# Kernel optimization log

Measured on AMD Instinct MI355X. Metric: run time of the kernel, lower is better.

The kernel has to match this reference:

```python
import jax, jax.numpy as jnp
import numpy as np


def setup_inputs() -> dict:
    key = jax.random.key(0)
    ks = jax.random.split(key, 5)
    B, T, S, D = 4, 32, 320, 768
    return {
        "x": jax.random.normal(ks[0], (B, T, S, D), dtype=jnp.float32),
        "qkv_w": jax.random.normal(ks[1], (D, 3 * D), dtype=jnp.float32) * 0.02,
        "qkv_b": jax.random.normal(ks[2], (3 * D,), dtype=jnp.float32) * 0.02,
        "out_w": jax.random.normal(ks[3], (D, D), dtype=jnp.float32) * 0.02,
        "out_b": jax.random.normal(ks[4], (D,), dtype=jnp.float32) * 0.02,
        "n_latents": 64,
        "n_heads": 12,
    }


def reference(x, qkv_w, qkv_b, out_w, out_b, n_latents, n_heads):
    B, T, S, D = x.shape
    H = n_heads
    hd = D // H
    scale = 1.0 / jnp.sqrt(jnp.asarray(hd, dtype=x.dtype))

    # qkv projection: [B,T,S,3D]
    qkv = jnp.einsum('btsd,de->btse', x, qkv_w) + qkv_b
    q, k, v = jnp.split(qkv, 3, axis=-1)
    # [B,T,S,H,hd]
    q = q.reshape(B, T, S, H, hd)
    k = k.reshape(B, T, S, H, hd)
    v = v.reshape(B, T, S, H, hd)

    # block-sparse mask: latent queries (rows < n_latents) cannot attend to
    # patch keys (cols >= n_latents); everything else allowed
    rows = jnp.arange(S) < n_latents          # latent query rows
    cols = jnp.arange(S) >= n_latents         # patch key cols
    allow = ~(rows[:, None] & cols[None, :])  # [S,S] bool

    # attention scores [B,T,H,Sq,Sk]
    scores = jnp.einsum('btqhd,btkhd->bthqk', q, k) * scale
    scores = jnp.where(allow, scores, -jnp.inf)
    attn = jax.nn.softmax(scores, axis=-1)

    y = jnp.einsum('bthqk,btkhd->btqhd', attn, v).reshape(B, T, S, D)
    return jnp.einsum('btsd,de->btse', y, out_w) + out_b
```

## Files before the change

### kernel.cpp

```cpp
#include <hip/hip_runtime.h>

typedef __attribute__((ext_vector_type(8))) short bf16x8;
typedef __attribute__((ext_vector_type(4))) float f32x4;
typedef __attribute__((ext_vector_type(16))) float f32x16;
typedef __attribute__((address_space(1))) void gvoid_t;
typedef __attribute__((address_space(3))) void lvoid_t;

#define DEVI __device__ __forceinline__

DEVI unsigned short f2bf(float f) {
    unsigned int u = __builtin_bit_cast(unsigned int, f);
    u += 0x7fffu + ((u >> 16) & 1u);
    return (unsigned short)(u >> 16);
}

DEVI unsigned cvt_pk_bf16(float a, float b) {
    unsigned r;
    asm("v_cvt_pk_bf16_f32 %0, %1, %2" : "=v"(r) : "v"(a), "v"(b));
    return r;
}

DEVI f32x4 mfma16(bf16x8 a, bf16x8 b, f32x4 c) {
    return __builtin_amdgcn_mfma_f32_16x16x32_bf16(a, b, c, 0, 0, 0);
}

__global__ void k_convert(const float* __restrict__ in, unsigned short* __restrict__ out, int n8) {
    int i = blockIdx.x * 256 + threadIdx.x;
    if (i >= n8) return;
    const float4* p = (const float4*)in + (size_t)i * 2;
    float4 a = p[0], b = p[1];
    uint4 o;
    o.x = f2bf(a.x) | ((unsigned)f2bf(a.y) << 16);
    o.y = f2bf(a.z) | ((unsigned)f2bf(a.w) << 16);
    o.z = f2bf(b.x) | ((unsigned)f2bf(b.y) << 16);
    o.w = f2bf(b.z) | ((unsigned)f2bf(b.w) << 16);
    *((uint4*)out + i) = o;
}

__global__ void k_transpose(const float* __restrict__ w, unsigned short* __restrict__ wt, int K, int N) {
    __shared__ float tile[32][33];
    int n0 = blockIdx.x * 32, k0 = blockIdx.y * 32;
    int tx = threadIdx.x, ty = threadIdx.y;
#pragma unroll
    for (int r = 0; r < 32; r += 8)
        tile[ty + r][tx] = w[(size_t)(k0 + ty + r) * N + n0 + tx];
    __syncthreads();
#pragma unroll
    for (int r = 0; r < 32; r += 8)
        wt[(size_t)(n0 + ty + r) * K + k0 + tx] = f2bf(tile[tx][ty + r]);
}

template <bool OUT_BF16>
__global__ __launch_bounds__(512, 2) void k_gemm256(const unsigned short* __restrict__ A,
                                                    const unsigned short* __restrict__ Bt,
                                                    const float* __restrict__ bias,
                                                    void* __restrict__ out,
                                                    int M, int N, int K) {
    __shared__ unsigned short smem[65536];

    const int tid = threadIdx.x;
    const int nwg = gridDim.x, bid = blockIdx.x;
    const int q8 = nwg >> 3, r8 = nwg & 7;
    const int xcd = bid & 7, lid = bid >> 3;
    const int swz = ((xcd < r8) ? xcd * (q8 + 1) : r8 * (q8 + 1) + (xcd - r8) * q8) + lid;
    const int ntn = N >> 8;
    const int bm = swz / ntn, bn = swz % ntn;

    const int lane = tid & 63, wid = tid >> 6;
    const int wr = wid >> 2, wc = wid & 3;
    const int lr = lane & 15, lg = lane >> 4;
    const int cswz = (lr & 7) << 3;
    const int col0 = (lg * 8) ^ cswz;

    const int NT = K >> 6;

    const int srowl = tid >> 3;
    const int scole = ((tid & 7) ^ (srowl & 7)) << 3;
    const unsigned short* aSrc = A  + (size_t)(bm * 256 + srowl) * K + scole;
    const unsigned short* bSrc = Bt + (size_t)(bn * 256 + srowl) * K + scole;

#define STG(matOff, srcBase, qq, koff, bufw)                                              \
    __builtin_amdgcn_global_load_lds((gvoid_t*)((srcBase) + (size_t)(qq) * 64 * K + (koff)), \
        (lvoid_t*)(smem + (matOff) + (bufw) * 16384 + (qq) * 4096 + tid * 8), 16, 0, 0)

    f32x4 acc[8][4];
#pragma unroll
    for (int i = 0; i < 8; ++i)
#pragma unroll
        for (int j = 0; j < 4; ++j) acc[i][j] = (f32x4){0.f, 0.f, 0.f, 0.f};

    {
        const int k1 = (NT > 1) ? 64 : 0;
        STG(0, aSrc, 0, 0, 0); STG(0, aSrc, 1, 0, 0); STG(0, aSrc, 2, 0, 0); STG(0, aSrc, 3, 0, 0);
        STG(32768, bSrc, 0, 0, 0); STG(32768, bSrc, 1, 0, 0); STG(32768, bSrc, 2, 0, 0); STG(32768, bSrc, 3, 0, 0);
        STG(0, aSrc, 0, k1, 1); STG(0, aSrc, 2, k1, 1);
        asm volatile("s_waitcnt vmcnt(2)" ::: "memory");
        __builtin_amdgcn_s_barrier();
    }

#pragma unroll 1
    for (int t = 0; t < NT; ++t) {
        const int bufR = t & 1, bufW = bufR ^ 1;
        const int ko1 = (t + 1 < NT) ? (t + 1) * 64 : 0;
        const int ko2 = (t + 2 < NT) ? (t + 2) * 64 : 0;
        const unsigned short* abuf = smem + bufR * 16384;
        const unsigned short* bbuf = smem + 32768 + bufR * 16384;
        bf16x8 af[4][2], bfr[2][2];

#pragma unroll
        for (int mf = 0; mf < 4; ++mf)
#pragma unroll
            for (int kk = 0; kk < 2; ++kk)
                af[mf][kk] = *(const bf16x8*)(abuf + (wr * 128 + mf * 16 + lr) * 64 + (col0 ^ (kk * 32)));
#pragma unroll
        for (int j = 0; j < 2; ++j)
#pragma unroll
            for (int kk = 0; kk < 2; ++kk)
                bfr[j][kk] = *(const bf16x8*)(bbuf + (wc * 64 + j * 16 + lr) * 64 + (col0 ^ (kk * 32)));
        STG(32768, bSrc, 0, ko1, bufW); STG(32768, bSrc, 1, ko1, bufW);
        __builtin_amdgcn_s_barrier();
        asm volatile("s_waitcnt lgkmcnt(0)" ::: "memory");
        __builtin_amdgcn_sched_barrier(0);
        __builtin_amdgcn_s_setprio(1);
#pragma unroll
        for (int mf = 0; mf < 4; ++mf)
#pragma unroll
            for (int j = 0; j < 2; ++j)
#pragma unroll
                for (int kk = 0; kk < 2; ++kk)
                    acc[mf][j] = mfma16(af[mf][kk], bfr[j][kk], acc[mf][j]);
        __builtin_amdgcn_s_setprio(0);
        __builtin_amdgcn_s_barrier();

#pragma unroll
        for (int j = 0; j < 2; ++j)
#pragma unroll
            for (int kk = 0; kk < 2; ++kk)
                bfr[j][kk] = *(const bf16x8*)(bbuf + (wc * 64 + (2 + j) * 16 + lr) * 64 + (col0 ^ (kk * 32)));
        STG(32768, bSrc, 2, ko1, bufW); STG(32768, bSrc, 3, ko1, bufW);
        __builtin_amdgcn_s_barrier();
        asm volatile("s_waitcnt lgkmcnt(0)" ::: "memory");
        __builtin_amdgcn_sched_barrier(0);
        __builtin_amdgcn_s_setprio(1);
#pragma unroll
        for (int mf = 0; mf < 4; ++mf)
#pragma unroll
            for (int j = 0; j < 2; ++j)
#pragma unroll
                for (int kk = 0; kk < 2; ++kk)
                    acc[mf][2 + j] = mfma16(af[mf][kk], bfr[j][kk], acc[mf][2 + j]);
        __builtin_amdgcn_s_setprio(0);
        __builtin_amdgcn_s_barrier();

#pragma unroll
        for (int mf = 0; mf < 4; ++mf)
#pragma unroll
            for (int kk = 0; kk < 2; ++kk)
                af[mf][kk] = *(const bf16x8*)(abuf + (wr * 128 + 64 + mf * 16 + lr) * 64 + (col0 ^ (kk * 32)));
        STG(0, aSrc, 1, ko1, bufW); STG(0, aSrc, 3, ko1, bufW);
        __builtin_amdgcn_s_barrier();
        asm volatile("s_waitcnt lgkmcnt(0)" ::: "memory");
        __builtin_amdgcn_sched_barrier(0);
        __builtin_amdgcn_s_setprio(1);
#pragma unroll
        for (int mf = 0; mf < 4; ++mf)
#pragma unroll
            for (int j = 0; j < 2; ++j)
#pragma unroll
                for (int kk = 0; kk < 2; ++kk)
                    acc[4 + mf][2 + j] = mfma16(af[mf][kk], bfr[j][kk], acc[4 + mf][2 + j]);
        __builtin_amdgcn_s_setprio(0);
        __builtin_amdgcn_s_barrier();

#pragma unroll
        for (int j = 0; j < 2; ++j)
#pragma unroll
            for (int kk = 0; kk < 2; ++kk)
                bfr[j][kk] = *(const bf16x8*)(bbuf + (wc * 64 + j * 16 + lr) * 64 + (col0 ^ (kk * 32)));
        STG(0, aSrc, 0, ko2, bufR); STG(0, aSrc, 2, ko2, bufR);
        __builtin_amdgcn_s_barrier();
        asm volatile("s_waitcnt lgkmcnt(0)" ::: "memory");
        __builtin_amdgcn_sched_barrier(0);
        __builtin_amdgcn_s_setprio(1);
#pragma unroll
        for (int mf = 0; mf < 4; ++mf)
#pragma unroll
            for (int j = 0; j < 2; ++j)
#pragma unroll
                for (int kk = 0; kk < 2; ++kk)
                    acc[4 + mf][j] = mfma16(af[mf][kk], bfr[j][kk], acc[4 + mf][j]);
        __builtin_amdgcn_s_setprio(0);
        asm volatile("s_waitcnt vmcnt(2)" ::: "memory");
        __builtin_amdgcn_s_barrier();
    }
#undef STG

#pragma unroll
    for (int mf = 0; mf < 8; ++mf)
#pragma unroll
        for (int nf = 0; nf < 4; ++nf) {
            int col = bn * 256 + wc * 64 + nf * 16 + lr;
            float bv = bias[col];
#pragma unroll
            for (int i = 0; i < 4; ++i) {
                int row = bm * 256 + wr * 128 + mf * 16 + lg * 4 + i;
                float v = acc[mf][nf][i] + bv;
                if (OUT_BF16)
                    ((unsigned short*)out)[(size_t)row * N + col] = f2bf(v);
                else
                    ((float*)out)[(size_t)row * N + col] = v;
            }
        }
}

__global__ __launch_bounds__(640) void k_attn2(const unsigned short* __restrict__ qkv,
                                               unsigned short* __restrict__ y) {
    int bt = blockIdx.x / 12, h = blockIdx.x % 12;
    const unsigned short* Qg = qkv + (size_t)bt * 320 * 2304 + h * 64;
    const unsigned short* Kg = Qg + 768;
    const unsigned short* Vg = Qg + 1536;

    __shared__ unsigned short Vt[64 * 40];

    int tid = threadIdx.x, w = tid >> 6, l = tid & 63;
    int q = l & 31, hh = l >> 5;
    int q0 = w * 32;
    int ntile = (w < 2) ? 2 : 10;

    bf16x8 qf[4];
#pragma unroll
    for (int c = 0; c < 4; ++c)
        qf[c] = *(const bf16x8*)(Qg + (size_t)(q0 + q) * 2304 + c * 16 + hh * 8);

    f32x16 o0 = (f32x16)0.f, o1 = (f32x16)0.f;
    float m = -3e38f, lsum = 0.f;
    const float SC = 0.125f * 1.44269504089f;

    for (int t = 0; t < 10; ++t) {
        if (tid < 512) {
            int sk = tid >> 4;
            int sd = (tid & 15) * 4;
            union { uint2 u; unsigned short s[4]; } vv;
            vv.u = *(const uint2*)(Vg + (size_t)(t * 32 + sk) * 2304 + sd);
#pragma unroll
            for (int j = 0; j < 4; ++j) {
                int d = sd + j;
                Vt[d * 40 + (sk ^ (((d >> 3) & 3) << 3))] = vv.s[j];
            }
        }
        __syncthreads();

        if (t < ntile) {
            int s0 = t * 32;
            bf16x8 kf[4];
#pragma unroll
            for (int c = 0; c < 4; ++c)
                kf[c] = *(const bf16x8*)(Kg + (size_t)(s0 + q) * 2304 + c * 16 + hh * 8);

            f32x16 sacc = (f32x16)0.f;
#pragma unroll
            for (int c = 0; c < 4; ++c)
                sacc = __builtin_amdgcn_mfma_f32_32x32x16_bf16(kf[c], qf[c], sacc, 0, 0, 0);

            float p[16];
            float tm = -3e38f;
#pragma unroll
            for (int r = 0; r < 16; ++r) {
                p[r] = sacc[r] * SC;
                tm = fmaxf(tm, p[r]);
            }
            tm = fmaxf(tm, __shfl_xor(tm, 32));
            if (!__all(tm <= m + 8.f)) {
                float mn = fmaxf(m, tm);
                float al = __builtin_amdgcn_exp2f(m - mn);
                lsum *= al;
#pragma unroll
                for (int r = 0; r < 16; ++r) { o0[r] *= al; o1[r] *= al; }
                m = mn;
            }
#pragma unroll
            for (int r = 0; r < 16; ++r) {
                p[r] = __builtin_amdgcn_exp2f(p[r] - m);
                lsum += p[r];
            }

            unsigned a0 = cvt_pk_bf16(p[0], p[1]);
            unsigned a1 = cvt_pk_bf16(p[2], p[3]);
            unsigned b0 = cvt_pk_bf16(p[4], p[5]);
            unsigned b1 = cvt_pk_bf16(p[6], p[7]);
            asm("v_permlane32_swap_b32 %0, %1" : "+v"(a0), "+v"(b0));
            asm("v_permlane32_swap_b32 %0, %1" : "+v"(a1), "+v"(b1));
            unsigned c0 = cvt_pk_bf16(p[8], p[9]);
            unsigned c1 = cvt_pk_bf16(p[10], p[11]);
            unsigned d0 = cvt_pk_bf16(p[12], p[13]);
            unsigned d1 = cvt_pk_bf16(p[14], p[15]);
            asm("v_permlane32_swap_b32 %0, %1" : "+v"(c0), "+v"(d0));
            asm("v_permlane32_swap_b32 %0, %1" : "+v"(c1), "+v"(d1));
            union { unsigned u[4]; bf16x8 v; } pf0, pf1;
            pf0.u[0] = a0; pf0.u[1] = a1; pf0.u[2] = b0; pf0.u[3] = b1;
            pf1.u[0] = c0; pf1.u[1] = c1; pf1.u[2] = d0; pf1.u[3] = d1;

            {
                int d = q;
                int sw = (d >> 3) & 3;
                bf16x8 va0 = *(const bf16x8*)&Vt[d * 40 + ((0 + hh) ^ sw) * 8];
                bf16x8 va1 = *(const bf16x8*)&Vt[d * 40 + ((2 + hh) ^ sw) * 8];
                o0 = __builtin_amdgcn_mfma_f32_32x32x16_bf16(va0, pf0.v, o0, 0, 0, 0);
                o0 = __builtin_amdgcn_mfma_f32_32x32x16_bf16(va1, pf1.v, o0, 0, 0, 0);
            }
            {
                int d = 32 + q;
                int sw = (d >> 3) & 3;
                bf16x8 va0 = *(const bf16x8*)&Vt[d * 40 + ((0 + hh) ^ sw) * 8];
                bf16x8 va1 = *(const bf16x8*)&Vt[d * 40 + ((2 + hh) ^ sw) * 8];
                o1 = __builtin_amdgcn_mfma_f32_32x32x16_bf16(va0, pf0.v, o1, 0, 0, 0);
                o1 = __builtin_amdgcn_mfma_f32_32x32x16_bf16(va1, pf1.v, o1, 0, 0, 0);
            }
        }
        __syncthreads();
    }

    lsum += __shfl_xor(lsum, 32);
    float inv = 1.f / lsum;
    unsigned short* yp = y + (size_t)(bt * 320 + q0 + q) * 768 + h * 64;
#pragma unroll
    for (int r = 0; r < 16; r += 2) {
        int dr = (r & 3) + 8 * (r >> 2) + 4 * hh;
        *(unsigned*)(yp + dr) =
            (unsigned)f2bf(o0[r] * inv) | ((unsigned)f2bf(o0[r + 1] * inv) << 16);
        *(unsigned*)(yp + 32 + dr) =
            (unsigned)f2bf(o1[r] * inv) | ((unsigned)f2bf(o1[r + 1] * inv) << 16);
    }
}

extern "C" void kernel_launch(void* const* d_in, const int* in_sizes, int n_in,
                              void* d_out, int out_size, void* d_ws, size_t ws_size,
                              hipStream_t stream) {
    const float* x     = (const float*)d_in[0];
    const float* qkv_w = (const float*)d_in[1];
    const float* qkv_b = (const float*)d_in[2];
    const float* out_w = (const float*)d_in[3];
    const float* out_b = (const float*)d_in[4];

    const int M = 40960;
    unsigned short* xb  = (unsigned short*)d_ws;
    unsigned short* w1t = xb + (size_t)M * 768;
    unsigned short* w2t = w1t + (size_t)2304 * 768;
    unsigned short* qkv = w2t + (size_t)768 * 768;
    unsigned short* yb  = qkv + (size_t)M * 2304;

    k_convert<<<(M * 768 / 8 + 255) / 256, 256, 0, stream>>>(x, xb, M * 768 / 8);
    k_transpose<<<dim3(2304 / 32, 768 / 32), dim3(32, 8), 0, stream>>>(qkv_w, w1t, 768, 2304);
    k_transpose<<<dim3(768 / 32, 768 / 32), dim3(32, 8), 0, stream>>>(out_w, w2t, 768, 768);

    k_gemm256<true><<<(M / 256) * (2304 / 256), 512, 0, stream>>>(xb, w1t, qkv_b, (void*)qkv, M, 2304, 768);
    k_attn2<<<128 * 12, 640, 0, stream>>>(qkv, yb);
    k_gemm256<false><<<(M / 256) * (768 / 256), 512, 0, stream>>>(yb, w2t, out_b, d_out, M, 768, 768);
}
```

Baseline: 438.7 us.

## Preload entire V head into LDS once, removing per-tile barriers in attention

The attention kernel now loads all 320 rows of V for the head into shared memory up front, transposed and swizzled, using 16-byte loads from all 640 threads. A single barrier replaces the two per-tile barriers, so each wave runs only its own number of tiles instead of stepping through all ten in lockstep. The max and sum reductions are rewritten as trees to shorten dependency chains. The cost is about 51KB of LDS per block, which may lower how many blocks fit on a CU.

```diff
diff --git a/kernel.cpp b/kernel.cpp
--- a/kernel.cpp
+++ b/kernel.cpp
@@ -213,20 +213,37 @@
         }
 }
 
-__global__ __launch_bounds__(640) void k_attn2(const unsigned short* __restrict__ qkv,
+__global__ __launch_bounds__(640) void k_attn3(const unsigned short* __restrict__ qkv,
                                                unsigned short* __restrict__ y) {
     int bt = blockIdx.x / 12, h = blockIdx.x % 12;
     const unsigned short* Qg = qkv + (size_t)bt * 320 * 2304 + h * 64;
     const unsigned short* Kg = Qg + 768;
     const unsigned short* Vg = Qg + 1536;
 
-    __shared__ unsigned short Vt[64 * 40];
+    __shared__ unsigned short Vt[10 * 64 * 40];
 
     int tid = threadIdx.x, w = tid >> 6, l = tid & 63;
     int q = l & 31, hh = l >> 5;
     int q0 = w * 32;
     int ntile = (w < 2) ? 2 : 10;
 
+    {
+        int k = tid >> 1;
+        int tt = k >> 5, sk = k & 31;
+        int d0 = (tid & 1) * 32;
+        const unsigned short* src = Vg + (size_t)k * 2304 + d0;
+#pragma unroll
+        for (int c = 0; c < 4; ++c) {
+            union { uint4 u; unsigned short s[8]; } vv;
+            vv.u = *(const uint4*)(src + c * 8);
+#pragma unroll
+            for (int j = 0; j < 8; ++j) {
+                int d = d0 + c * 8 + j;
+                Vt[(tt * 64 + d) * 40 + (sk ^ (((d >> 3) & 3) << 3))] = vv.s[j];
+            }
+        }
+    }
+
     bf16x8 qf[4];
 #pragma unroll
     for (int c = 0; c < 4; ++c)
@@ -236,88 +253,77 @@
     float m = -3e38f, lsum = 0.f;
     const float SC = 0.125f * 1.44269504089f;
 
-    for (int t = 0; t < 10; ++t) {
-        if (tid < 512) {
-            int sk = tid >> 4;
-            int sd = (tid & 15) * 4;
-            union { uint2 u; unsigned short s[4]; } vv;
-            vv.u = *(const uint2*)(Vg + (size_t)(t * 32 + sk) * 2304 + sd);
-#pragma unroll
-            for (int j = 0; j < 4; ++j) {
-                int d = sd + j;
-                Vt[d * 40 + (sk ^ (((d >> 3) & 3) << 3))] = vv.s[j];
-            }
-        }
-        __syncthreads();
-
-        if (t < ntile) {
-            int s0 = t * 32;
-            bf16x8 kf[4];
-#pragma unroll
-            for (int c = 0; c < 4; ++c)
-                kf[c] = *(const bf16x8*)(Kg + (size_t)(s0 + q) * 2304 + c * 16 + hh * 8);
-
-            f32x16 sacc = (f32x16)0.f;
-#pragma unroll
-            for (int c = 0; c < 4; ++c)
-                sacc = __builtin_amdgcn_mfma_f32_32x32x16_bf16(kf[c], qf[c], sacc, 0, 0, 0);
-
-            float p[16];
-            float tm = -3e38f;
-#pragma unroll
-            for (int r = 0; r < 16; ++r) {
-                p[r] = sacc[r] * SC;
-                tm = fmaxf(tm, p[r]);
-            }
-            tm = fmaxf(tm, __shfl_xor(tm, 32));
-            if (!__all(tm <= m + 8.f)) {
-                float mn = fmaxf(m, tm);
-                float al = __builtin_amdgcn_exp2f(m - mn);
-                lsum *= al;
-#pragma unroll
-                for (int r = 0; r < 16; ++r) { o0[r] *= al; o1[r] *= al; }
-                m = mn;
-            }
-#pragma unroll
-            for (int r = 0; r < 16; ++r) {
-                p[r] = __builtin_amdgcn_exp2f(p[r] - m);
-                lsum += p[r];
-            }
-
-            unsigned a0 = cvt_pk_bf16(p[0], p[1]);
-            unsigned a1 = cvt_pk_bf16(p[2], p[3]);
-            unsigned b0 = cvt_pk_bf16(p[4], p[5]);
-            unsigned b1 = cvt_pk_bf16(p[6], p[7]);
-            asm("v_permlane32_swap_b32 %0, %1" : "+v"(a0), "+v"(b0));
-            asm("v_permlane32_swap_b32 %0, %1" : "+v"(a1), "+v"(b1));
-            unsigned c0 = cvt_pk_bf16(p[8], p[9]);
-            unsigned c1 = cvt_pk_bf16(p[10], p[11]);
-            unsigned d0 = cvt_pk_bf16(p[12], p[13]);
-            unsigned d1 = cvt_pk_bf16(p[14], p[15]);
-            asm("v_permlane32_swap_b32 %0, %1" : "+v"(c0), "+v"(d0));
-            asm("v_permlane32_swap_b32 %0, %1" : "+v"(c1), "+v"(d1));
-            union { unsigned u[4]; bf16x8 v; } pf0, pf1;
-            pf0.u[0] = a0; pf0.u[1] = a1; pf0.u[2] = b0; pf0.u[3] = b1;
-            pf1.u[0] = c0; pf1.u[1] = c1; pf1.u[2] = d0; pf1.u[3] = d1;
-
-            {
-                int d = q;
-                int sw = (d >> 3) & 3;
-                bf16x8 va0 = *(const bf16x8*)&Vt[d * 40 + ((0 + hh) ^ sw) * 8];
-                bf16x8 va1 = *(const bf16x8*)&Vt[d * 40 + ((2 + hh) ^ sw) * 8];
-                o0 = __builtin_amdgcn_mfma_f32_32x32x16_bf16(va0, pf0.v, o0, 0, 0, 0);
-                o0 = __builtin_amdgcn_mfma_f32_32x32x16_bf16(va1, pf1.v, o0, 0, 0, 0);
-            }
-            {
-                int d = 32 + q;
-                int sw = (d >> 3) & 3;
-                bf16x8 va0 = *(const bf16x8*)&Vt[d * 40 + ((0 + hh) ^ sw) * 8];
-                bf16x8 va1 = *(const bf16x8*)&Vt[d * 40 + ((2 + hh) ^ sw) * 8];
-                o1 = __builtin_amdgcn_mfma_f32_32x32x16_bf16(va0, pf0.v, o1, 0, 0, 0);
-                o1 = __builtin_amdgcn_mfma_f32_32x32x16_bf16(va1, pf1.v, o1, 0, 0, 0);
-            }
-        }
-        __syncthreads();
+    __syncthreads();
+
+    for (int t = 0; t < ntile; ++t) {
+        int s0 = t * 32;
+        bf16x8 kf[4];
+#pragma unroll
+        for (int c = 0; c < 4; ++c)
+            kf[c] = *(const bf16x8*)(Kg + (size_t)(s0 + q) * 2304 + c * 16 + hh * 8);
+
+        f32x16 sacc = (f32x16)0.f;
+#pragma unroll
+        for (int c = 0; c < 4; ++c)
+            sacc = __builtin_amdgcn_mfma_f32_32x32x16_bf16(kf[c], qf[c], sacc, 0, 0, 0);
+
+        float p[16];
+#pragma unroll
+        for (int r = 0; r < 16; ++r) p[r] = sacc[r] * SC;
+        float tm = fmaxf(
+            fmaxf(fmaxf(fmaxf(p[0], p[1]), fmaxf(p[2], p[3])),
+                  fmaxf(fmaxf(p[4], p[5]), fmaxf(p[6], p[7]))),
+            fmaxf(fmaxf(fmaxf(p[8], p[9]), fmaxf(p[10], p[11])),
+                  fmaxf(fmaxf(p[12], p[13]), fmaxf(p[14], p[15]))));
+        tm = fmaxf(tm, __shfl_xor(tm, 32));
+        if (!__all(tm <= m + 8.f)) {
+            float mn = fmaxf(m, tm);
+            float al = __builtin_amdgcn_exp2f(m - mn);
+            lsum *= al;
+#pragma unroll
+            for (int r = 0; r < 16; ++r) { o0[r] *= al; o1[r] *= al; }
+            m = mn;
+        }
+#pragma unroll
+        for (int r = 0; r < 16; ++r) p[r] = __builtin_amdgcn_exp2f(p[r] - m);
+        float rs =
+            ((p[0] + p[1]) + (p[2] + p[3])) + ((p[4] + p[5]) + (p[6] + p[7])) +
+            (((p[8] + p[9]) + (p[10] + p[11])) + ((p[12] + p[13]) + (p[14] + p[15])));
+        lsum += rs;
+
+        unsigned a0 = cvt_pk_bf16(p[0], p[1]);
+        unsigned a1 = cvt_pk_bf16(p[2], p[3]);
+        unsigned b0 = cvt_pk_bf16(p[4], p[5]);
+        unsigned b1 = cvt_pk_bf16(p[6], p[7]);
+        asm("v_permlane32_swap_b32 %0, %1" : "+v"(a0), "+v"(b0));
+        asm("v_permlane32_swap_b32 %0, %1" : "+v"(a1), "+v"(b1));
+        unsigned c0 = cvt_pk_bf16(p[8], p[9]);
+        unsigned c1 = cvt_pk_bf16(p[10], p[11]);
+        unsigned d0 = cvt_pk_bf16(p[12], p[13]);
+        unsigned d1 = cvt_pk_bf16(p[14], p[15]);
+        asm("v_permlane32_swap_b32 %0, %1" : "+v"(c0), "+v"(d0));
+        asm("v_permlane32_swap_b32 %0, %1" : "+v"(c1), "+v"(d1));
+        union { unsigned u[4]; bf16x8 v; } pf0, pf1;
+        pf0.u[0] = a0; pf0.u[1] = a1; pf0.u[2] = b0; pf0.u[3] = b1;
+        pf1.u[0] = c0; pf1.u[1] = c1; pf1.u[2] = d0; pf1.u[3] = d1;
+
+        const unsigned short* vt = Vt + t * 2560;
+        {
+            int d = q;
+            int sw = (d >> 3) & 3;
+            bf16x8 va0 = *(const bf16x8*)&vt[d * 40 + ((0 + hh) ^ sw) * 8];
+            bf16x8 va1 = *(const bf16x8*)&vt[d * 40 + ((2 + hh) ^ sw) * 8];
+            o0 = __builtin_amdgcn_mfma_f32_32x32x16_bf16(va0, pf0.v, o0, 0, 0, 0);
+            o0 = __builtin_amdgcn_mfma_f32_32x32x16_bf16(va1, pf1.v, o0, 0, 0, 0);
+        }
+        {
+            int d = 32 + q;
+            int sw = (d >> 3) & 3;
+            bf16x8 va0 = *(const bf16x8*)&vt[d * 40 + ((0 + hh) ^ sw) * 8];
+            bf16x8 va1 = *(const bf16x8*)&vt[d * 40 + ((2 + hh) ^ sw) * 8];
+            o1 = __builtin_amdgcn_mfma_f32_32x32x16_bf16(va0, pf0.v, o1, 0, 0, 0);
+            o1 = __builtin_amdgcn_mfma_f32_32x32x16_bf16(va1, pf1.v, o1, 0, 0, 0);
+        }
     }
 
     lsum += __shfl_xor(lsum, 32);
@@ -354,6 +360,6 @@
     k_transpose<<<dim3(768 / 32, 768 / 32), dim3(32, 8), 0, stream>>>(out_w, w2t, 768, 768);
 
     k_gemm256<true><<<(M / 256) * (2304 / 256), 512, 0, stream>>>(xb, w1t, qkv_b, (void*)qkv, M, 2304, 768);
-    k_attn2<<<128 * 12, 640, 0, stream>>>(qkv, yb);
+    k_attn3<<<128 * 12, 640, 0, stream>>>(qkv, yb);
     k_gemm256<false><<<(M / 256) * (768 / 256), 512, 0, stream>>>(yb, w2t, out_b, d_out, M, 768, 768);
 }
```

Result: faster. 381.9 us (-12.9%).
